# Kernel tuning notes

Measured on AMD Instinct MI355X. Metric: run time of the kernel, lower is better.

## Reference

```python
import jax, jax.numpy as jnp
import numpy as np
from jax import lax

# ASiM CIM-simulation constants (stand-in for cfg.asim_vit_mlp_*)
XBIT = 4        # activation bits (signed, two's complement)
WBIT = 4        # weight bits (signed, two's complement)
NROW = 256      # crossbar rows per partition
ADC_PREC = 8    # ADC precision bits


def _ste_round(v):
    return v + lax.stop_gradient(jnp.round(v) - v)


def _quant_signed(x, bits):
    qmax = float(2 ** (bits - 1) - 1)
    scale = jnp.maximum(jnp.max(jnp.abs(x)) / qmax, 1e-8)
    q = jnp.clip(_ste_round(x / scale), -(qmax + 1.0), qmax)
    return q, scale  # q holds integers as float32


def _cim_matmul(x_q, w_q):
    """Bit-serial analog CIM matmul with row partitioning + ADC truncation.
    x_q: [N, Din] signed ints (float), w_q: [Dout, Din] signed ints (float).
    Returns integer-domain result [N, Dout]."""
    N, Din = x_q.shape
    Dout = w_q.shape[0]
    nseg = -(-Din // NROW)
    pad = nseg * NROW - Din
    x3 = jnp.pad(x_q, ((0, 0), (0, pad))).reshape(N, nseg, NROW)
    w3 = jnp.pad(w_q, ((0, 0), (0, pad))).reshape(Dout, nseg, NROW)
    # two's complement bit planes
    xtc = jnp.mod(x3, 2 ** XBIT)
    wtc = jnp.mod(w3, 2 ** WBIT)
    step = NROW / float(2 ** ADC_PREC)
    levels = float(2 ** ADC_PREC - 1)
    acc = jnp.zeros((N, Dout), dtype=x_q.dtype)
    for i in range(XBIT):
        xb = jnp.mod(jnp.floor(xtc / (2 ** i)), 2.0)  # [N, nseg, NROW] in {0,1}
        si = -1.0 if i == XBIT - 1 else 1.0           # MSB has negative weight
        for j in range(WBIT):
            wb = jnp.mod(jnp.floor(wtc / (2 ** j)), 2.0)
            sj = -1.0 if j == WBIT - 1 else 1.0
            psum = jnp.einsum('nsk,osk->nso', xb, wb)  # per-partition analog sum
            psum = jnp.clip(jnp.round(psum / step), 0.0, levels) * step  # ADC
            acc = acc + (si * sj * (2 ** (i + j))) * psum.sum(axis=1)
    return acc


def _asim_linear(x, w, b):
    """x: [..., Din]; w: [Dout, Din]; b: [Dout]. Forward = CIM simulated value;
    gradient path = STE-quantized ideal matmul."""
    sh = x.shape
    x2 = x.reshape(-1, sh[-1])
    xq, sx = _quant_signed(x2, XBIT)
    wq, sw = _quant_signed(w, WBIT)
    ideal = (xq @ wq.T) * (sx * sw)
    cim = _cim_matmul(lax.stop_gradient(xq), lax.stop_gradient(wq)) * lax.stop_gradient(sx * sw)
    out = ideal + lax.stop_gradient(cim - ideal) + b
    return out.reshape(sh[:-1] + (w.shape[0],))


def setup_inputs() -> dict:
    key = jax.random.key(0)
    ks = jax.random.split(key, 5)
    B, S, D, H = 16, 197, 768, 3072
    x = jax.random.normal(ks[0], (B, S, D), dtype=jnp.float32)
    w1 = jax.random.normal(ks[1], (H, D), dtype=jnp.float32) * (1.0 / np.sqrt(D))
    b1 = jax.random.normal(ks[2], (H,), dtype=jnp.float32) * 0.01
    w2 = jax.random.normal(ks[3], (D, H), dtype=jnp.float32) * (1.0 / np.sqrt(H))
    b2 = jax.random.normal(ks[4], (D,), dtype=jnp.float32) * 0.01
    return {"x": x, "w1": w1, "b1": b1, "w2": w2, "b2": b2}


def reference(x, w1, b1, w2, b2):
    h = _asim_linear(x, w1, b1)
    h = jax.nn.gelu(h, approximate=False)  # torch nn.GELU default (erf)
    # dropout p=0.0 -> identity
    out = _asim_linear(h, w2, b2)
    return out
```

## Files before the change

### kernel.cpp

```cpp
#include <hip/hip_runtime.h>
#include <hip/hip_bf16.h>
#include <stdint.h>

typedef int i32x4 __attribute__((ext_vector_type(4)));

#define GLL(gp, lp) __builtin_amdgcn_global_load_lds( \
    (const __attribute__((address_space(1))) void*)(gp), \
    (__attribute__((address_space(3))) void*)(lp), 16, 0, 0)


__device__ __forceinline__ float xla_erf(float x) {
#pragma clang fp contract(off)
  x = fminf(3.832506856900711f, fmaxf(-3.832506856900711f, x));
  float x2 = x * x;
  float p = -2.72614225801306e-10f;
  p = p * x2 + 2.77068142495902e-08f;
  p = p * x2 + -2.10102402082508e-06f;
  p = p * x2 + -5.69250639462346e-05f;
  p = p * x2 + -7.34990630326855e-04f;
  p = p * x2 + -2.95459980854025e-03f;
  p = p * x2 + -1.60960333262415e-02f;
  p = x * p;
  float q = -1.45660718464996e-05f;
  q = q * x2 + -2.13374055278905e-04f;
  q = q * x2 + -1.68282697438203e-03f;
  q = q * x2 + -7.37332916720468e-03f;
  q = q * x2 + -1.42647390514189e-02f;
  return p / q;
}

__device__ __forceinline__ float gelu_exact(float x) {
#pragma clang fp contract(off)
  float t = x / 1.41421356237309504880f;
  float e = xla_erf(t);
  float u = e + 1.0f;
  float v = x * u;
  return v * 0.5f;
}

__device__ __forceinline__ float epi_scale(float iacc, float sc, float b) {
#pragma clang fp contract(off)
  float v = iacc * sc;
  v = v + b;
  return v;
}

__device__ __forceinline__ int quant1(float x, float scale) {
#pragma clang fp contract(off)
  float t = x / scale;
  t = rintf(t);
  t = fmaxf(-8.0f, fminf(7.0f, t));
  return (int)t;
}

__device__ __forceinline__ long tiled_off(long m, long c, int kt) {
  return (((m >> 4) * kt + (c >> 6)) << 10) +
         ((((m & 15) | (((c >> 4) & 3) << 4))) << 4) + (c & 15);
}


__global__ void init_kernel(unsigned* slots) {
  if (threadIdx.x < 4) slots[threadIdx.x] = 0u;
}

__global__ void absmax3(const float* __restrict__ p0, long n0,
                        const float* __restrict__ p1, long n1,
                        const float* __restrict__ p2, long n2,
                        unsigned* __restrict__ slots) {
  __shared__ float red[4];
  const int t = blockIdx.y;
  const float4* p = (const float4*)(t == 0 ? p0 : (t == 1 ? p1 : p2));
  const long n4 = (t == 0 ? n0 : (t == 1 ? n1 : n2));
  float m = 0.0f;
  long i = (long)blockIdx.x * blockDim.x + threadIdx.x;
  const long stride = (long)gridDim.x * blockDim.x;
  for (; i < n4; i += stride) {
    float4 v = p[i];
    m = fmaxf(m, fmaxf(fmaxf(fabsf(v.x), fabsf(v.y)), fmaxf(fabsf(v.z), fabsf(v.w))));
  }
  for (int o = 32; o > 0; o >>= 1) m = fmaxf(m, __shfl_xor(m, o));
  if ((threadIdx.x & 63) == 0) red[threadIdx.x >> 6] = m;
  __syncthreads();
  if (threadIdx.x == 0) {
    m = fmaxf(fmaxf(red[0], red[1]), fmaxf(red[2], red[3]));
    atomicMax(slots + t, __float_as_uint(m));
  }
}

__global__ void quant3(const float* __restrict__ in0, const float* __restrict__ in1,
                       const float* __restrict__ in2,
                       int Rp0, int Rp1, int Rp2, int R0, int R1, int R2,
                       int C0, int C1, int C2, int kt0, int kt1, int kt2,
                       const unsigned* __restrict__ slots,
                       char* __restrict__ o0, char* __restrict__ o1,
                       char* __restrict__ o2) {
  const int y = blockIdx.y;
  const float* in = (y == 0 ? in0 : (y == 1 ? in1 : in2));
  char* qout = (y == 0 ? o0 : (y == 1 ? o1 : o2));
  const int Rpad = (y == 0 ? Rp0 : (y == 1 ? Rp1 : Rp2));
  const int R = (y == 0 ? R0 : (y == 1 ? R1 : R2));
  const int C = (y == 0 ? C0 : (y == 1 ? C1 : C2));
  const int kt = (y == 0 ? kt0 : (y == 1 ? kt1 : kt2));
  const int sign = (y == 0 ? 1 : -1);
  const int segs_per_row = C >> 8;
  const int seg = blockIdx.x * 4 + (threadIdx.x >> 6);
  if (seg >= Rpad * segs_per_row) return;
  const int lane = threadIdx.x & 63;
  const int r = seg / segs_per_row;
  const int s = seg - r * segs_per_row;
  const float scale = fmaxf(__uint_as_float(slots[y]) / 7.0f, 1e-8f);
  const long n = (long)s * 256 + lane * 4;
  int mask = 0;
  unsigned pk = 0u;
  if (r < R) {
    const size_t base = (size_t)r * C + n;
    float4 v = *(const float4*)(in + base);
    int q0 = quant1(v.x, scale);
    int q1 = quant1(v.y, scale);
    int q2 = quant1(v.z, scale);
    int q3 = quant1(v.w, scale);
    pk = (q0 & 0xff) | ((q1 & 0xff) << 8) | ((q2 & 0xff) << 16) |
         ((unsigned)(q3 & 0xff) << 24);
    mask = q0 & q1 & q2 & q3 & 15;
  }
  *(unsigned*)(qout + tiled_off(r, n, kt)) = pk;
  for (int o = 32; o > 0; o >>= 1) mask &= __shfl_xor(mask, o);
  if (lane == 0)
    qout[tiled_off(r, C + s, kt)] = (char)(sign * ((mask & 7) - (mask & 8)));
  const int padw = kt * 64 - C - segs_per_row;
  if (s == 0 && lane < padw)
    qout[tiled_off(r, C + segs_per_row + lane, kt)] = 0;
}

template <int MODE>
__global__ __launch_bounds__(256) void gemm_frag(
    const char* __restrict__ A, const char* __restrict__ B,
    int ktA, int mtiles, int kbase, int krem,
    i32x4* __restrict__ frag, long cslots,
    const float* __restrict__ bias, const unsigned* __restrict__ slots,
    int Mstore, float* __restrict__ pmax) {
  __shared__ char Abuf[3][4096];
  __shared__ char Bbuf[3][4096];
  const int tid = threadIdx.x;
  const int lane = tid & 63;
  const int wv = tid >> 6;

  const int nwg = gridDim.x;
  const int q8 = nwg >> 3, r8 = nwg & 7;
  const int xcd = blockIdx.x & 7, idx = blockIdx.x >> 3;
  const int sw = (xcd < r8 ? xcd * (q8 + 1) : r8 * (q8 + 1) + (xcd - r8) * q8) + idx;
  const int bm = sw % mtiles;
  const int bn = sw / mtiles;
  const long m0 = (long)bm * 64;
  const long n0 = (long)bn * 64;
  const int chunk = blockIdx.y;
  const int k_begin = chunk * kbase + min(chunk, krem);
  const int k_iters = kbase + (chunk < krem ? 1 : 0);

  const int wm = wv >> 1, wn = wv & 1;
  const int lr = lane & 15, kg = lane >> 4;

  const char* gA = A + (((long)(m0 >> 4) + wv) * ktA + k_begin) * 1024 + lane * 16;
  const char* gB = B + (((long)(n0 >> 4) + wv) * ktA + k_begin) * 1024 + lane * 16;

#define STAGE(buf, kk) do { \
    GLL(gA + (long)(kk) * 1024, (char*)Abuf + (buf) * 4096 + wv * 1024); \
    GLL(gB + (long)(kk) * 1024, (char*)Bbuf + (buf) * 4096 + wv * 1024); \
  } while (0)

  i32x4 acc[2][2] = {};

  STAGE(0, 0);
  if (k_iters > 1) STAGE(1, 1);
  int cur = 0;
  for (int kt = 0; kt < k_iters; ++kt) {
    if (kt + 2 < k_iters) {
      const int nb = cur == 0 ? 2 : (cur == 1 ? 0 : 1);
      STAGE(nb, kt + 2);
      asm volatile("s_waitcnt vmcnt(4)" ::: "memory");
    } else if (kt + 1 < k_iters) {
      asm volatile("s_waitcnt vmcnt(2)" ::: "memory");
    } else {
      asm volatile("s_waitcnt vmcnt(0)" ::: "memory");
    }
    __builtin_amdgcn_s_barrier();
    const char* pa = (const char*)Abuf + cur * 4096;
    const char* pb = (const char*)Bbuf + cur * 4096;
    i32x4 av[2], bv[2];
#pragma unroll
    for (int f = 0; f < 2; ++f)
      av[f] = *(const i32x4*)(pa + (wm * 2 + f) * 1024 + lane * 16);
#pragma unroll
    for (int f = 0; f < 2; ++f)
      bv[f] = *(const i32x4*)(pb + (wn * 2 + f) * 1024 + lane * 16);
#pragma unroll
    for (int fa = 0; fa < 2; ++fa)
#pragma unroll
      for (int fb = 0; fb < 2; ++fb)
        acc[fa][fb] = __builtin_amdgcn_mfma_i32_16x16x64_i8(av[fa], bv[fb], acc[fa][fb], 0, 0, 0);
    __builtin_amdgcn_s_barrier();
    cur = cur == 2 ? 0 : cur + 1;
  }
#undef STAGE

  i32x4* po = frag + (long)chunk * cslots + (((long)sw * 4 + wv) * 4) * 64 + lane;

  if (MODE == 0) {
    __shared__ float red[4];
    const float sa = fmaxf(__uint_as_float(slots[0]) / 7.0f, 1e-8f);
    const float sb = fmaxf(__uint_as_float(slots[1]) / 7.0f, 1e-8f);
    const float sc = sa * sb;
    float bl[2];
#pragma unroll
    for (int fb = 0; fb < 2; ++fb) bl[fb] = bias[n0 + wn * 32 + fb * 16 + lr];
    float hmax = 0.0f;
#pragma unroll
    for (int fa = 0; fa < 2; ++fa) {
#pragma unroll
      for (int fb = 0; fb < 2; ++fb) {
        float4 g;
#pragma unroll
        for (int rr = 0; rr < 4; ++rr) {
          float h = gelu_exact(epi_scale((float)acc[fa][fb][rr], sc, bl[fb]));
          (&g.x)[rr] = h;
          const long m = m0 + wm * 32 + fa * 16 + kg * 4 + rr;
          if (m < Mstore) hmax = fmaxf(hmax, fabsf(h));
        }
        *(float4*)(po + (fa * 2 + fb) * 64) = g;
      }
    }
    for (int o = 32; o > 0; o >>= 1) hmax = fmaxf(hmax, __shfl_xor(hmax, o));
    if ((tid & 63) == 0) red[tid >> 6] = hmax;
    __syncthreads();
    if (tid == 0)
      pmax[blockIdx.x] = fmaxf(fmaxf(red[0], red[1]), fmaxf(red[2], red[3]));
  } else {
#pragma unroll
    for (int fa = 0; fa < 2; ++fa)
#pragma unroll
      for (int fb = 0; fb < 2; ++fb)
        po[(fa * 2 + fb) * 64] = acc[fa][fb];
  }
}

__global__ void epi1max_final(const float* __restrict__ pmax, int n,
                              unsigned* __restrict__ slots) {
  __shared__ float red[4];
  float m = 0.0f;
  for (int i = threadIdx.x; i < n; i += 256) m = fmaxf(m, pmax[i]);
  for (int o = 32; o > 0; o >>= 1) m = fmaxf(m, __shfl_xor(m, o));
  if ((threadIdx.x & 63) == 0) red[threadIdx.x >> 6] = m;
  __syncthreads();
  if (threadIdx.x == 0)
    slots[3] = __float_as_uint(fmaxf(fmaxf(red[0], red[1]), fmaxf(red[2], red[3])));
}

__global__ __launch_bounds__(256) void quant_h(
    const float* __restrict__ gfrag, int mtiles, int Mstore,
    const unsigned* __restrict__ slots, char* __restrict__ hqt) {
  __shared__ unsigned char lds_m[24][16];
  const int rt = blockIdx.x >> 1;
  const int half = blockIdx.x & 1;
  const int tid = threadIdx.x;
  const int lane = tid & 63, w = tid >> 6;
  const int kg = lane >> 4, lr = lane & 15;
  const float sh = fmaxf(__uint_as_float(slots[3]) / 7.0f, 1e-8f);
  const int bm = rt >> 2, wm = (rt >> 1) & 1, fa = rt & 1;
  const long mrow0 = (long)rt * 16 + kg * 4;

  for (int j = 0; j < 6; ++j) {
    const int bnl = w + 4 * j;
    const int bn = half * 24 + bnl;
    int rowmask[4] = {15, 15, 15, 15};
#pragma unroll
    for (int wn = 0; wn < 2; ++wn) {
#pragma unroll
      for (int fb = 0; fb < 2; ++fb) {
        const long slot = (((long)bn * mtiles + bm) * 4 + (wm * 2 + wn)) * 4 +
                          (fa * 2 + fb);
        float4 v = ((const float4*)gfrag)[slot * 64 + lane];
#pragma unroll
        for (int rr = 0; rr < 4; ++rr) {
          const long m = mrow0 + rr;
          int q = 0;
          if (m < Mstore) q = quant1((&v.x)[rr], sh);
          hqt[((long)rt * 49 + bn) * 1024 +
              (((kg * 4 + rr) | ((wn * 2 + fb) << 4)) << 4) + lr] = (char)q;
          rowmask[rr] &= (q & 15);
        }
      }
    }
#pragma unroll
    for (int rr = 0; rr < 4; ++rr) {
      rowmask[rr] &= __shfl_xor(rowmask[rr], 1);
      rowmask[rr] &= __shfl_xor(rowmask[rr], 2);
      rowmask[rr] &= __shfl_xor(rowmask[rr], 4);
      rowmask[rr] &= __shfl_xor(rowmask[rr], 8);
    }
    if (lr == 0) {
#pragma unroll
      for (int rr = 0; rr < 4; ++rr)
        lds_m[bnl][kg * 4 + rr] = (unsigned char)rowmask[rr];
    }
  }
  __syncthreads();
  if (tid < 96) {
    const int sl = tid >> 4, row = tid & 15;
    int m8 = lds_m[sl * 4][row] & lds_m[sl * 4 + 1][row] &
             lds_m[sl * 4 + 2][row] & lds_m[sl * 4 + 3][row] & 15;
    const int gs = half * 6 + sl;
    hqt[tiled_off((long)rt * 16 + row, 3072 + gs, 49)] =
        (char)((m8 & 7) - (m8 & 8));
  }
  if (half == 1) {
    for (int t = tid; t < 52 * 16; t += 256) {
      const int col = 3084 + (t >> 4), row = t & 15;
      hqt[tiled_off((long)rt * 16 + row, col, 49)] = 0;
    }
  }
}

struct Dec { long mb; long n; };
__device__ __forceinline__ Dec frag_decode(long t, int mtiles) {
  const int slot = (int)(t >> 10);
  const int r = (int)t & 1023;
  const int wv = r >> 8, fafb = (r >> 6) & 3, lane = r & 63;
  const int fa = fafb >> 1, fb = fafb & 1;
  const int wm = wv >> 1, wn = wv & 1;
  const int kg = lane >> 4, lr = lane & 15;
  const int bm = slot % mtiles, bn = slot / mtiles;
  Dec d;
  d.mb = (long)bm * 64 + wm * 32 + fa * 16 + kg * 4;
  d.n = (long)bn * 64 + wn * 32 + fb * 16 + lr;
  return d;
}

__global__ void epi2frag(const i32x4* __restrict__ frag, long cslots, int mtiles,
                         int Mstore, const float* __restrict__ b2,
                         const unsigned* __restrict__ slots,
                         float* __restrict__ out, int ldo) {
  const long t = (long)blockIdx.x * 256 + threadIdx.x;
  if (t >= cslots) return;
  const float sa = fmaxf(__uint_as_float(slots[3]) / 7.0f, 1e-8f);
  const float sb = fmaxf(__uint_as_float(slots[2]) / 7.0f, 1e-8f);
  const float sc = sa * sb;
  Dec d = frag_decode(t, mtiles);
  i32x4 c0 = frag[t];
  i32x4 c1 = frag[t + cslots];
  i32x4 c2 = frag[t + 2 * cslots];
  i32x4 c3 = frag[t + 3 * cslots];
  const float b = b2[d.n];
#pragma unroll
  for (int rr = 0; rr < 4; ++rr) {
    const long m = d.mb + rr;
    if (m < Mstore) {
      int s = (c0[rr] + c1[rr]) + (c2[rr] + c3[rr]);
      out[m * (long)ldo + d.n] = epi_scale((float)s, sc, b);
    }
  }
}


extern "C" void kernel_launch(void* const* d_in, const int* in_sizes, int n_in,
                              void* d_out, int out_size, void* d_ws, size_t ws_size,
                              hipStream_t stream) {
  const float* x  = (const float*)d_in[0];
  const float* w1 = (const float*)d_in[1];
  const float* b1 = (const float*)d_in[2];
  const float* w2 = (const float*)d_in[3];
  const float* b2 = (const float*)d_in[4];
  float* out = (float*)d_out;

  const int Ntok = 16 * 197;
  const int Mpad = 3328;
  const int D = 768, H = 3072;
  const int KT1 = 13;
  const int KT2 = 49;
  const int SPLITK = 4;
  const int MT = Mpad / 64;
  const int NB1 = MT * (H / 64);
  const long NF1 = (long)NB1 * 1024;
  const long CS2 = (long)MT * (D / 64) * 1024;

  char* ws = (char*)d_ws;
  size_t o = 0;
  unsigned* slots = (unsigned*)(ws + o); o += 256;
  float* pmax = (float*)(ws + o); o += 16384;
  char* xqt  = ws + o; o += (size_t)(Mpad / 16) * KT1 * 1024;
  char* wq1t = ws + o; o += (size_t)(H / 16) * KT1 * 1024;
  char* wq2t = ws + o; o += (size_t)(D / 16) * KT2 * 1024;
  char* hqt  = ws + o; o += (size_t)(Mpad / 16) * KT2 * 1024;
  o = (o + 1023) & ~(size_t)1023;
  i32x4* frag = (i32x4*)(ws + o); o += (size_t)NF1 * 16;
  (void)ws_size; (void)in_sizes; (void)n_in; (void)out_size;

  hipLaunchKernelGGL(init_kernel, dim3(1), dim3(64), 0, stream, slots);

  hipLaunchKernelGGL(absmax3, dim3(512, 3), dim3(256), 0, stream,
                     x, (long)Ntok * D / 4, w1, (long)H * D / 4,
                     w2, (long)D * H / 4, slots);

  hipLaunchKernelGGL(quant3, dim3(Mpad * (D / 256) / 4, 3), dim3(256), 0, stream,
                     x, w1, w2, Mpad, H, D, Ntok, H, D, D, D, H,
                     KT1, KT1, KT2, slots, xqt, wq1t, wq2t);

  hipLaunchKernelGGL((gemm_frag<0>), dim3(NB1, 1), dim3(256), 0, stream,
                     xqt, wq1t, KT1, MT, KT1, 0, frag, 0L,
                     b1, slots, Ntok, pmax);
  hipLaunchKernelGGL(epi1max_final, dim3(1), dim3(256), 0, stream,
                     pmax, NB1, slots);

  hipLaunchKernelGGL(quant_h, dim3((Mpad / 16) * 2), dim3(256), 0, stream,
                     (const float*)frag, MT, Ntok, slots, hqt);

  hipLaunchKernelGGL((gemm_frag<1>), dim3(MT * (D / 64), SPLITK), dim3(256), 0, stream,
                     hqt, wq2t, KT2, MT, KT2 / SPLITK, KT2 % SPLITK, frag, CS2,
                     nullptr, nullptr, 0, nullptr);

  hipLaunchKernelGGL(epi2frag, dim3((unsigned)(CS2 / 256)), dim3(256), 0, stream,
                     frag, CS2, MT, Ntok, b2, slots, out, D);
}
```

Before: 126.2 us.

## Switch GEMM to double buffering and fold max reduction into quant_h

The GEMM main loop now uses a two-stage LDS ring instead of three, prefetching one tile ahead with unroll 2. This cuts LDS footprint and removes the modulo-3 buffer bookkeeping, at the cost of less latency hiding for the global-to-LDS loads. Separately, the single-block epi1max_final kernel is removed and every quant_h block reduces the per-block maxima itself, saving one launch but repeating that small reduction in every block.

```diff
diff --git a/kernel.cpp b/kernel.cpp
--- a/kernel.cpp
+++ b/kernel.cpp
@@ -139,8 +139,8 @@
     i32x4* __restrict__ frag, long cslots,
     const float* __restrict__ bias, const unsigned* __restrict__ slots,
     int Mstore, float* __restrict__ pmax) {
-  __shared__ char Abuf[3][4096];
-  __shared__ char Bbuf[3][4096];
+  __shared__ char Abuf[2][4096];
+  __shared__ char Bbuf[2][4096];
   const int tid = threadIdx.x;
   const int lane = tid & 63;
   const int wv = tid >> 6;
@@ -171,35 +171,29 @@
   i32x4 acc[2][2] = {};
 
   STAGE(0, 0);
-  if (k_iters > 1) STAGE(1, 1);
-  int cur = 0;
+#pragma unroll 2
   for (int kt = 0; kt < k_iters; ++kt) {
-    if (kt + 2 < k_iters) {
-      const int nb = cur == 0 ? 2 : (cur == 1 ? 0 : 1);
-      STAGE(nb, kt + 2);
-      asm volatile("s_waitcnt vmcnt(4)" ::: "memory");
-    } else if (kt + 1 < k_iters) {
+    const int cur = kt & 1;
+    if (kt + 1 < k_iters) {
+      STAGE(cur ^ 1, kt + 1);
       asm volatile("s_waitcnt vmcnt(2)" ::: "memory");
     } else {
       asm volatile("s_waitcnt vmcnt(0)" ::: "memory");
     }
     __builtin_amdgcn_s_barrier();
-    const char* pa = (const char*)Abuf + cur * 4096;
-    const char* pb = (const char*)Bbuf + cur * 4096;
     i32x4 av[2], bv[2];
 #pragma unroll
     for (int f = 0; f < 2; ++f)
-      av[f] = *(const i32x4*)(pa + (wm * 2 + f) * 1024 + lane * 16);
+      av[f] = *(const i32x4*)(Abuf[cur] + (wm * 2 + f) * 1024 + lane * 16);
 #pragma unroll
     for (int f = 0; f < 2; ++f)
-      bv[f] = *(const i32x4*)(pb + (wn * 2 + f) * 1024 + lane * 16);
+      bv[f] = *(const i32x4*)(Bbuf[cur] + (wn * 2 + f) * 1024 + lane * 16);
 #pragma unroll
     for (int fa = 0; fa < 2; ++fa)
 #pragma unroll
       for (int fb = 0; fb < 2; ++fb)
         acc[fa][fb] = __builtin_amdgcn_mfma_i32_16x16x64_i8(av[fa], bv[fb], acc[fa][fb], 0, 0, 0);
     __builtin_amdgcn_s_barrier();
-    cur = cur == 2 ? 0 : cur + 1;
   }
 #undef STAGE
 
@@ -243,28 +237,28 @@
   }
 }
 
-__global__ void epi1max_final(const float* __restrict__ pmax, int n,
-                              unsigned* __restrict__ slots) {
-  __shared__ float red[4];
-  float m = 0.0f;
-  for (int i = threadIdx.x; i < n; i += 256) m = fmaxf(m, pmax[i]);
-  for (int o = 32; o > 0; o >>= 1) m = fmaxf(m, __shfl_xor(m, o));
-  if ((threadIdx.x & 63) == 0) red[threadIdx.x >> 6] = m;
-  __syncthreads();
-  if (threadIdx.x == 0)
-    slots[3] = __float_as_uint(fmaxf(fmaxf(red[0], red[1]), fmaxf(red[2], red[3])));
-}
-
 __global__ __launch_bounds__(256) void quant_h(
     const float* __restrict__ gfrag, int mtiles, int Mstore,
-    const unsigned* __restrict__ slots, char* __restrict__ hqt) {
+    const float* __restrict__ pmax, int nb,
+    unsigned* __restrict__ slots, char* __restrict__ hqt) {
   __shared__ unsigned char lds_m[24][16];
+  __shared__ float red[4];
+  const int tid = threadIdx.x;
+  const int lane = tid & 63, w = tid >> 6;
+
+  float gm = 0.0f;
+  for (int i = tid; i < nb; i += 256) gm = fmaxf(gm, pmax[i]);
+  for (int o = 32; o > 0; o >>= 1) gm = fmaxf(gm, __shfl_xor(gm, o));
+  if (lane == 0) red[w] = gm;
+  __syncthreads();
+  gm = fmaxf(fmaxf(red[0], red[1]), fmaxf(red[2], red[3]));
+  if (blockIdx.x == 0 && tid == 0) slots[3] = __float_as_uint(gm);
+  const float sh = fmaxf(gm / 7.0f, 1e-8f);
+  __syncthreads();
+
   const int rt = blockIdx.x >> 1;
   const int half = blockIdx.x & 1;
-  const int tid = threadIdx.x;
-  const int lane = tid & 63, w = tid >> 6;
   const int kg = lane >> 4, lr = lane & 15;
-  const float sh = fmaxf(__uint_as_float(slots[3]) / 7.0f, 1e-8f);
   const int bm = rt >> 2, wm = (rt >> 1) & 1, fa = rt & 1;
   const long mrow0 = (long)rt * 16 + kg * 4;
 
@@ -407,11 +401,9 @@
   hipLaunchKernelGGL((gemm_frag<0>), dim3(NB1, 1), dim3(256), 0, stream,
                      xqt, wq1t, KT1, MT, KT1, 0, frag, 0L,
                      b1, slots, Ntok, pmax);
-  hipLaunchKernelGGL(epi1max_final, dim3(1), dim3(256), 0, stream,
-                     pmax, NB1, slots);
 
   hipLaunchKernelGGL(quant_h, dim3((Mpad / 16) * 2), dim3(256), 0, stream,
-                     (const float*)frag, MT, Ntok, slots, hqt);
+                     (const float*)frag, MT, Ntok, pmax, NB1, slots, hqt);
 
   hipLaunchKernelGGL((gemm_frag<1>), dim3(MT * (D / 64), SPLITK), dim3(256), 0, stream,
                      hqt, wq2t, KT2, MT, KT2 / SPLITK, KT2 % SPLITK, frag, CS2,
```

After: 123.1 us. 1.02x faster.
